# Optimization experiments

Hardware: AMD Instinct MI355X
Metric: run time of the kernel (lower is better)

The kernel has to match this reference:

```python
import jax, jax.numpy as jnp
import numpy as np

K = 16          # nsample (ball-query neighbors via topk smallest sqdist)
EPS = 1e-5      # BatchNorm eps


def conv1(x, W, b):
    # pointwise Conv1d (kernel=1): x [B,N,Cin], W [Cout,Cin], b [Cout] -> [B,N,Cout]
    return jnp.einsum('bnc,oc->bno', x, W) + b


def bn_train(x, gamma, beta):
    # BatchNorm1d in training mode: stats over batch and length dims
    mean = jnp.mean(x, axis=(0, 1))
    var = jnp.var(x, axis=(0, 1))
    return (x - mean) * jax.lax.rsqrt(var + EPS) * gamma + beta


def farthest_point_sample(xyz, npoint):
    # xyz [B,N,3] -> idx [B,npoint]; deterministic start at index 0
    B, N, _ = xyz.shape

    def step(carry, _):
        dist, far = carry                                        # [B,N], [B]
        centroid = jnp.take_along_axis(xyz, far[:, None, None], axis=1)  # [B,1,3]
        d = jnp.sum((xyz - centroid) ** 2, axis=-1)              # [B,N]
        dist = jnp.minimum(dist, d)
        nxt = jnp.argmax(dist, axis=1).astype(jnp.int32)
        return (dist, nxt), far

    init = (jnp.full((B, N), jnp.finfo(xyz.dtype).max, xyz.dtype),
            jnp.zeros((B,), jnp.int32))
    _, idx = jax.lax.scan(step, init, None, length=npoint)       # [npoint,B]
    return idx.T                                                  # [B,npoint]


def sqdist(a, b):
    # a [B,S,3], b [B,N,3] -> [B,S,N]
    return (jnp.sum(a ** 2, -1)[:, :, None]
            + jnp.sum(b ** 2, -1)[:, None, :]
            - 2.0 * jnp.einsum('bsc,bnc->bsn', a, b))


def gather_groups(pc, idx):
    # pc [B,N,D], idx [B,S,K] -> [B,S,K,D]
    return jax.vmap(lambda p, i: p[i])(pc, idx)


def setup_inputs() -> dict:
    key = jax.random.key(0)
    ks = jax.random.split(key, 8)
    B, N = 8, 4096
    mid, out, cin = 32, 64, 3
    s = lambda fan: 1.0 / np.sqrt(fan)
    return {
        'x_in': jax.random.normal(ks[0], (B, N, cin), jnp.float32),
        'W1': jax.random.normal(ks[1], (mid, cin), jnp.float32) * s(cin),
        'b1': jnp.zeros((mid,), jnp.float32),
        'g1': jnp.ones((mid,), jnp.float32),
        'be1': jnp.zeros((mid,), jnp.float32),
        'W2': jax.random.normal(ks[2], (out, mid), jnp.float32) * s(mid),
        'b2': jnp.zeros((out,), jnp.float32),
        'W3': jax.random.normal(ks[3], (out, out + cin), jnp.float32) * s(out + cin),
        'b3': jnp.zeros((out,), jnp.float32),
        'g2': jnp.ones((out,), jnp.float32),
        'be2': jnp.zeros((out,), jnp.float32),
        'W4': jax.random.normal(ks[4], (out, out), jnp.float32) * s(out),
        'b4': jnp.zeros((out,), jnp.float32),
    }


def reference(x_in, W1, b1, g1, be1, W2, b2, W3, b3, g2, be2, W4, b4):
    B, N, C = x_in.shape
    S = N // 2
    # first_mlp: Conv1d -> BN -> ReLU -> Conv1d (all pointwise)
    h = jax.nn.relu(bn_train(conv1(x_in, W1, b1), g1, be1))
    feats = conv1(h, W2, b2)                                  # [B,N,64]
    # sample_and_group(npoint=N//2, nsample=K, xyz=x_in, points=feats)
    fps_idx = farthest_point_sample(x_in, S)                  # [B,S]
    new_xyz = jnp.take_along_axis(x_in, fps_idx[..., None], axis=1)  # [B,S,3]
    d = sqdist(new_xyz, x_in)                                 # [B,S,N]
    _, idx = jax.lax.top_k(-d, K)                             # [B,S,K] smallest dists
    grouped_xyz = gather_groups(x_in, idx) - new_xyz[:, :, None, :]  # [B,S,K,3]
    grouped_pts = gather_groups(feats, idx)                   # [B,S,K,64]
    x_cat = jnp.concatenate([grouped_xyz, grouped_pts], axis=-1)  # [B,S,K,67]
    pooled = jnp.max(x_cat, axis=2)                           # [B,S,67]
    # last_mlp
    h = jax.nn.relu(bn_train(conv1(pooled, W3, b3), g2, be2))
    return conv1(h, W4, b4)                                   # [B,S,64]
```

## Files before the change

### kernel.cpp

```cpp
#include <hip/hip_runtime.h>
#include <float.h>

#define BB   8
#define NN   4096
#define SS   2048
#define MID  32
#define COUT 64
#define CAT  67
#define M1   (BB*NN)
#define M2   (BB*SS)
#define EPSB 1e-5f
#define NCHUNK 64
#define CSZ    32

#define I_B0   0
#define I_B1   16
#define I_B2   32
#define I_TKT  64
#define I_PROG 80
#define WS_RED2  256
#define WS_RED1  400
#define WS_FPS   1024
#define WS_FEATS (1024 + 16384)
#define WS_POOL  (WS_FEATS + M1*COUT)

struct SA  { float red[8][9]; };
struct SB4 { float4 Pc[NN]; alignas(16) unsigned long long sv[2][8]; };
struct SB3 { float W1s[96]; float abv[64]; float W2s[2048]; float b2s[64]; float mom[9]; };
struct SC  { float4 Pq[NN]; unsigned long long cand[CSZ][257]; int fin[CSZ][16];
             float W3s[64 * CAT]; float b3s[64]; float ps[128]; int tkt; };
struct SE  { float W3t[CAT * 64]; float W4s[4096]; float b3s[64]; float b4s[64]; float ab[128]; };
union  SU  { SA a; SB4 b4; SB3 b3; SC c; SE e; };

__device__ __forceinline__ unsigned long long u64max(unsigned long long a,
                                                     unsigned long long b) {
    return a > b ? a : b;
}

template <int CTRL>
__device__ __forceinline__ unsigned long long dpp_swap_max(unsigned long long v) {
    int lo = (int)(unsigned)v;
    int hi = (int)(unsigned)(v >> 32);
    int olo = __builtin_amdgcn_update_dpp(0, lo, CTRL, 0xF, 0xF, false);
    int ohi = __builtin_amdgcn_update_dpp(0, hi, CTRL, 0xF, 0xF, false);
    unsigned long long ov = ((unsigned long long)(unsigned)ohi << 32) | (unsigned)olo;
    return u64max(v, ov);
}

__device__ __forceinline__ void barrier_join(int* ctr, int target) {
    __syncthreads();
    if (threadIdx.x == 0) {
        __threadfence();
        atomicAdd(ctr, 1);
        while (__hip_atomic_load(ctr, __ATOMIC_RELAXED, __HIP_MEMORY_SCOPE_AGENT) < target)
            __builtin_amdgcn_s_sleep(64);
        __threadfence();
    }
    __syncthreads();
}

__device__ __forceinline__ void top16_insert(unsigned long long* cv,
                                             unsigned long long newv,
                                             unsigned long long& cmaxv, int& cpos) {
#pragma unroll
    for (int j = 0; j < 16; j++) cv[j] = (j == cpos) ? newv : cv[j];
    unsigned long long m1a[8]; int p1a[8];
#pragma unroll
    for (int j = 0; j < 8; j++) {
        bool s = cv[2 * j + 1] > cv[2 * j];
        m1a[j] = s ? cv[2 * j + 1] : cv[2 * j];
        p1a[j] = s ? 2 * j + 1 : 2 * j;
    }
    unsigned long long m2a[4]; int p2a[4];
#pragma unroll
    for (int j = 0; j < 4; j++) {
        bool s = m1a[2 * j + 1] > m1a[2 * j];
        m2a[j] = s ? m1a[2 * j + 1] : m1a[2 * j];
        p2a[j] = s ? p1a[2 * j + 1] : p1a[2 * j];
    }
    unsigned long long m3a, m3b; int p3a, p3b;
    { bool s = m2a[1] > m2a[0]; m3a = s ? m2a[1] : m2a[0]; p3a = s ? p2a[1] : p2a[0]; }
    { bool s = m2a[3] > m2a[2]; m3b = s ? m2a[3] : m2a[2]; p3b = s ? p2a[3] : p2a[2]; }
    bool s = m3b > m3a;
    cmaxv = s ? m3b : m3a; cpos = s ? p3b : p3a;
}

__global__ __launch_bounds__(512) void fused(
        const float* __restrict__ xin,
        const float* __restrict__ W1, const float* __restrict__ b1,
        const float* __restrict__ g1, const float* __restrict__ be1,
        const float* __restrict__ W2, const float* __restrict__ b2,
        const float* __restrict__ W3, const float* __restrict__ b3,
        const float* __restrict__ g2, const float* __restrict__ be2,
        const float* __restrict__ W4, const float* __restrict__ b4,
        float* __restrict__ ws, float* __restrict__ out) {
    __shared__ SU sm;
    int blk = blockIdx.x, tid = threadIdx.x;
    int* ctri  = (int*)ws;
    int* fidxg = (int*)(ws + WS_FPS);
    (void)b1;

    if (blk < 8) {
        int b = blk;
        const float* xb = xin + (size_t)b * NN * 3;
        int* fob = fidxg + b * SS;
        int* progb = ctri + I_PROG + b * 16;
        float px[8], py[8], pz[8], dist[8];
#pragma unroll
        for (int k = 0; k < 8; k++) {
            int i = tid + (k << 9);
            float x = xb[3 * i], y = xb[3 * i + 1], z = xb[3 * i + 2];
            px[k] = x; py[k] = y; pz[k] = z; dist[k] = FLT_MAX;
            sm.b4.Pc[i] = make_float4(x, y, z, 0.f);
        }
        __syncthreads();
        float4 c0 = sm.b4.Pc[0];
        float cx = c0.x, cy = c0.y, cz = c0.z;
        int wid = tid >> 6, lane = tid & 63;
        int rbuf[8];
        rbuf[0] = 0;
        for (int t = 1; t < SS; t++) {
            float bv = -1.f; int bi = 0;
#pragma unroll
            for (int k = 0; k < 8; k++) {
                float dx = px[k] - cx, dy = py[k] - cy, dz = pz[k] - cz;
                float d = fmaf(dz, dz, fmaf(dy, dy, dx * dx));
                float nd = fminf(dist[k], d);
                dist[k] = nd;
                bool bt = nd > bv;
                bv = bt ? nd : bv; bi = bt ? (tid + (k << 9)) : bi;
            }
            unsigned long long v =
                ((unsigned long long)__float_as_uint(bv) << 32) | (unsigned)(~bi);
            v = dpp_swap_max<0xB1>(v);
            v = dpp_swap_max<0x4E>(v);
            v = dpp_swap_max<0x141>(v);
            v = dpp_swap_max<0x140>(v);
            {
                int a16 = ((lane ^ 16) << 2), a32 = ((lane ^ 32) << 2), a48 = ((lane ^ 48) << 2);
                int lo = (int)(unsigned)v, hi = (int)(unsigned)(v >> 32);
                int lo16 = __builtin_amdgcn_ds_bpermute(a16, lo);
                int hi16 = __builtin_amdgcn_ds_bpermute(a16, hi);
                int lo32 = __builtin_amdgcn_ds_bpermute(a32, lo);
                int hi32 = __builtin_amdgcn_ds_bpermute(a32, hi);
                int lo48 = __builtin_amdgcn_ds_bpermute(a48, lo);
                int hi48 = __builtin_amdgcn_ds_bpermute(a48, hi);
                unsigned long long v16 = ((unsigned long long)(unsigned)hi16 << 32) | (unsigned)lo16;
                unsigned long long v32 = ((unsigned long long)(unsigned)hi32 << 32) | (unsigned)lo32;
                unsigned long long v48 = ((unsigned long long)(unsigned)hi48 << 32) | (unsigned)lo48;
                v = u64max(u64max(v, v16), u64max(v32, v48));
            }
            int par = t & 1;
            if (lane == 0) sm.b4.sv[par][wid] = v;
            __syncthreads();
            const ulonglong2* sp = (const ulonglong2*)sm.b4.sv[par];
            ulonglong2 q0 = sp[0], q1 = sp[1], q2 = sp[2], q3 = sp[3];
            unsigned long long m0 = u64max(q0.x, q0.y), m1 = u64max(q1.x, q1.y);
            unsigned long long m2 = u64max(q2.x, q2.y), m3 = u64max(q3.x, q3.y);
            unsigned long long best = u64max(u64max(m0, m1), u64max(m2, m3));
            int bsel = (int)(~(unsigned)best);
            float4 cc = sm.b4.Pc[bsel];
            cx = cc.x; cy = cc.y; cz = cc.z;
            if (tid == 0) {
                rbuf[t & 7] = bsel;
                if ((t & 7) == 7) {
                    *(int4*)(fob + t - 7) = make_int4(rbuf[0], rbuf[1], rbuf[2], rbuf[3]);
                    *(int4*)(fob + t - 3) = make_int4(rbuf[4], rbuf[5], rbuf[6], rbuf[7]);
                    if ((t & 31) == 31)
                        __hip_atomic_store(progb, t + 1, __ATOMIC_RELEASE,
                                           __HIP_MEMORY_SCOPE_AGENT);
                }
            }
        }
        barrier_join(ctri + I_B2, 256);
    } else {
        if (blk < 72) {
            int p = (blk - 8) * 512 + tid;
            float x0 = xin[3 * p], x1 = xin[3 * p + 1], x2 = xin[3 * p + 2];
            float r[9];
            r[0] = x0; r[1] = x1; r[2] = x2;
            r[3] = x0 * x0; r[4] = x0 * x1; r[5] = x0 * x2;
            r[6] = x1 * x1; r[7] = x1 * x2; r[8] = x2 * x2;
#pragma unroll
            for (int m = 32; m; m >>= 1) {
#pragma unroll
                for (int q = 0; q < 9; q++) r[q] += __shfl_down(r[q], m, 64);
            }
            if ((tid & 63) == 0) {
#pragma unroll
                for (int q = 0; q < 9; q++) sm.a.red[tid >> 6][q] = r[q];
            }
            __syncthreads();
            if (tid == 0) {
#pragma unroll
                for (int q = 0; q < 9; q++) {
                    float s = 0.f;
#pragma unroll
                    for (int w = 0; w < 8; w++) s += sm.a.red[w][q];
                    ws[WS_RED1 + (blk - 8) * 9 + q] = s;
                }
            }
            barrier_join(ctri + I_B0, 64);
            for (int j = tid; j < 96; j += 512) sm.b3.W1s[j] = W1[j];
            if (tid < 64) sm.b3.b2s[tid] = b2[tid];
            for (int j = tid; j < 2048; j += 512) sm.b3.W2s[j] = W2[j];
            if (tid < 9) {
                float s = 0.f;
                for (int k = 0; k < 64; k++) s += ws[WS_RED1 + k * 9 + tid];
                sm.b3.mom[tid] = s;
            }
            __syncthreads();
            if (tid < MID) {
                float S0 = sm.b3.mom[0], S1 = sm.b3.mom[1], S2 = sm.b3.mom[2];
                float C00 = sm.b3.mom[3], C01 = sm.b3.mom[4], C02 = sm.b3.mom[5];
                float C11 = sm.b3.mom[6], C12 = sm.b3.mom[7], C22 = sm.b3.mom[8];
                float w0 = W1[3 * tid], w1 = W1[3 * tid + 1], w2 = W1[3 * tid + 2];
                float invM = 1.f / (float)M1;
                float meanc = (w0 * S0 + w1 * S1 + w2 * S2) * invM;
                float wCw = w0 * w0 * C00 + w1 * w1 * C11 + w2 * w2 * C22 +
                            2.f * (w0 * w1 * C01 + w0 * w2 * C02 + w1 * w2 * C12);
                float var = wCw * invM - meanc * meanc;
                float a = g1[tid] * rsqrtf(var + EPSB);
                sm.b3.abv[tid] = a;
                sm.b3.abv[MID + tid] = be1[tid] - meanc * a;
            }
            __syncthreads();
            int p2 = (blk - 8) * 512 + tid;
            float y0 = xin[3 * p2], y1 = xin[3 * p2 + 1], y2 = xin[3 * p2 + 2];
            float h[MID];
#pragma unroll
            for (int o = 0; o < MID; o++) {
                float y = fmaf(sm.b3.W1s[3 * o + 2], y2,
                         fmaf(sm.b3.W1s[3 * o + 1], y1, sm.b3.W1s[3 * o] * y0));
                h[o] = fmaxf(0.f, fmaf(sm.b3.abv[o], y, sm.b3.abv[MID + o]));
            }
            float* fo = ws + WS_FEATS + (size_t)p2 * COUT;
#pragma unroll
            for (int j = 0; j < COUT; j += 4) {
                float a0 = sm.b3.b2s[j], a1v = sm.b3.b2s[j + 1];
                float a2v = sm.b3.b2s[j + 2], a3v = sm.b3.b2s[j + 3];
#pragma unroll
                for (int o = 0; o < MID; o++) {
                    float hv = h[o];
                    a0  = fmaf(sm.b3.W2s[(j)     * MID + o], hv, a0);
                    a1v = fmaf(sm.b3.W2s[(j + 1) * MID + o], hv, a1v);
                    a2v = fmaf(sm.b3.W2s[(j + 2) * MID + o], hv, a2v);
                    a3v = fmaf(sm.b3.W2s[(j + 3) * MID + o], hv, a3v);
                }
                *(float4*)(fo + j) = make_float4(a0, a1v, a2v, a3v);
            }
        }
        barrier_join(ctri + I_B1, 248);

        for (int j = tid; j < 64 * CAT; j += 512) sm.c.W3s[j] = W3[j];
        if (tid < 64) sm.c.b3s[tid] = b3[tid];
        if (tid < 128) sm.c.ps[tid] = 0.f;
        __syncthreads();
        int c0ch = (tid & 15) * 4;
        float bsum[4] = {0.f, 0.f, 0.f, 0.f}, bsq[4] = {0.f, 0.f, 0.f, 0.f};
        int curb = -1;
        for (;;) {
            if (tid == 0) sm.c.tkt = atomicAdd(ctri + I_TKT, 1);
            __syncthreads();
            int tk = sm.c.tkt;
            if (tk >= BB * NCHUNK) break;
            int b = tk & 7, c = tk >> 3;
            if (b != curb) {
                const float* xb = xin + (size_t)b * NN * 3;
                for (int j = tid; j < NN; j += 512) {
                    float x = xb[3 * j], y = xb[3 * j + 1], z = xb[3 * j + 2];
                    sm.c.Pq[j] = make_float4(x, y, z, (x * x + y * y) + z * z);
                }
                curb = b;
            }
            if (tid == 0) {
                int* progb = ctri + I_PROG + b * 16;
                int need = (c + 1) * CSZ;
                while (__hip_atomic_load(progb, __ATOMIC_RELAXED,
                                         __HIP_MEMORY_SCOPE_AGENT) < need)
                    __builtin_amdgcn_s_sleep(64);
                (void)__hip_atomic_load(progb, __ATOMIC_ACQUIRE,
                                        __HIP_MEMORY_SCOPE_AGENT);
            }
            __syncthreads();
            int cc = tid >> 4, q = tid & 15;
            int s = c * CSZ + cc;
            int sg = b * SS + s;
            int ci = fidxg[sg];
            float4 cen = sm.c.Pq[ci];
            float an = cen.w;
            unsigned long long cv[16];
#pragma unroll
            for (int j = 0; j < 16; j++) cv[j] = ~0ULL;
            unsigned long long cmaxv = ~0ULL; int cpos = 0;
            for (int n0 = 0; n0 < 256; n0++) {
                int n = (q << 8) + ((n0 + q) & 255);
                float4 qq = sm.c.Pq[n];
                float dot = fmaf(cen.z, qq.z, fmaf(cen.y, qq.y, cen.x * qq.x));
                float dd = (an + qq.w) - 2.f * dot;
                unsigned db = __float_as_uint(dd);
                db ^= (unsigned)(((int)db >> 31) | 0x80000000u);
                unsigned long long newv = ((unsigned long long)db << 32) | (unsigned)n;
                if (newv < cmaxv) top16_insert(cv, newv, cmaxv, cpos);
            }
#pragma unroll
            for (int j = 0; j < 16; j++) sm.c.cand[cc][q * 16 + j] = cv[j];
            __syncthreads();
            if (tid < CSZ) {
                unsigned long long mv[16];
#pragma unroll
                for (int j = 0; j < 16; j++) mv[j] = ~0ULL;
                unsigned long long mx = ~0ULL; int mp = 0;
                for (int k = 0; k < 256; k++) {
                    unsigned long long e = sm.c.cand[tid][k];
                    if (e < mx) top16_insert(mv, e, mx, mp);
                }
#pragma unroll
                for (int j = 0; j < 16; j++) sm.c.fin[tid][j] = (int)(unsigned)mv[j];
            }
            __syncthreads();
            int idxs[16];
#pragma unroll
            for (int j = 0; j < 16; j++) idxs[j] = sm.c.fin[cc][j];
            const float* feats = ws + WS_FEATS + (size_t)b * NN * COUT;
            float4 acc = make_float4(-FLT_MAX, -FLT_MAX, -FLT_MAX, -FLT_MAX);
#pragma unroll 4
            for (int k = 0; k < 16; k++) {
                const float4* fp = (const float4*)(feats + (size_t)idxs[k] * COUT) + q;
                float4 v0 = fp[0];
                acc.x = fmaxf(acc.x, v0.x); acc.y = fmaxf(acc.y, v0.y);
                acc.z = fmaxf(acc.z, v0.z); acc.w = fmaxf(acc.w, v0.w);
            }
            float* po = ws + WS_POOL + (size_t)sg * CAT;
            po[3 + q * 4] = acc.x; po[4 + q * 4] = acc.y;
            po[5 + q * 4] = acc.z; po[6 + q * 4] = acc.w;
            if (q == 0) {
                float rx = -FLT_MAX, ry = -FLT_MAX, rz = -FLT_MAX;
#pragma unroll
                for (int k = 0; k < 16; k++) {
                    float4 p = sm.c.Pq[idxs[k]];
                    rx = fmaxf(rx, p.x - cen.x);
                    ry = fmaxf(ry, p.y - cen.y);
                    rz = fmaxf(rz, p.z - cen.z);
                }
                po[0] = rx; po[1] = ry; po[2] = rz;
            }
            __syncthreads();
            {
                int rrow = b * SS + c * CSZ + (tid >> 4);
                const float* rp = ws + WS_POOL + (size_t)rrow * CAT;
                float y0 = sm.c.b3s[c0ch],     y1 = sm.c.b3s[c0ch + 1];
                float y2 = sm.c.b3s[c0ch + 2], y3 = sm.c.b3s[c0ch + 3];
                for (int j = 0; j < CAT; j++) {
                    float pj = rp[j];
                    y0 = fmaf(sm.c.W3s[(c0ch)     * CAT + j], pj, y0);
                    y1 = fmaf(sm.c.W3s[(c0ch + 1) * CAT + j], pj, y1);
                    y2 = fmaf(sm.c.W3s[(c0ch + 2) * CAT + j], pj, y2);
                    y3 = fmaf(sm.c.W3s[(c0ch + 3) * CAT + j], pj, y3);
                }
                bsum[0] += y0; bsq[0] = fmaf(y0, y0, bsq[0]);
                bsum[1] += y1; bsq[1] = fmaf(y1, y1, bsq[1]);
                bsum[2] += y2; bsq[2] = fmaf(y2, y2, bsq[2]);
                bsum[3] += y3; bsq[3] = fmaf(y3, y3, bsq[3]);
            }
        }
#pragma unroll
        for (int u = 0; u < 4; u++) {
            atomicAdd(&sm.c.ps[c0ch + u], bsum[u]);
            atomicAdd(&sm.c.ps[64 + c0ch + u], bsq[u]);
        }
        __syncthreads();
        if (tid < 128) atomicAdd(ws + WS_RED2 + tid, sm.c.ps[tid]);
        barrier_join(ctri + I_B2, 256);
    }

    {
        for (int lin = tid; lin < CAT * 64; lin += 512) {
            int j = lin >> 6, o = lin & 63;
            sm.e.W3t[lin] = W3[o * CAT + j];
        }
        for (int j = tid; j < 4096; j += 512) sm.e.W4s[j] = W4[j];
        if (tid < 64) {
            sm.e.b3s[tid] = b3[tid]; sm.e.b4s[tid] = b4[tid];
            float inv = 1.f / (float)M2;
            float mean = ws[WS_RED2 + tid] * inv;
            float var = ws[WS_RED2 + 64 + tid] * inv - mean * mean;
            float a = g2[tid] * rsqrtf(var + EPSB);
            sm.e.ab[tid] = a;
            sm.e.ab[64 + tid] = be2[tid] - mean * a;
        }
        __syncthreads();
        if (tid < 64) {
            int pt = blk * 64 + tid;
            const float* row = ws + WS_POOL + (size_t)pt * CAT;
            float h[64];
#pragma unroll
            for (int c = 0; c < 64; c++) h[c] = sm.e.b3s[c];
            for (int j = 0; j < CAT; j++) {
                float pj = row[j];
#pragma unroll
                for (int c = 0; c < 64; c++) h[c] = fmaf(sm.e.W3t[j * 64 + c], pj, h[c]);
            }
#pragma unroll
            for (int c = 0; c < 64; c++)
                h[c] = fmaxf(0.f, fmaf(sm.e.ab[c], h[c], sm.e.ab[64 + c]));
            float* op = out + (size_t)pt * 64;
            for (int o = 0; o < 64; o += 4) {
                float a0 = sm.e.b4s[o], a1v = sm.e.b4s[o + 1];
                float a2v = sm.e.b4s[o + 2], a3v = sm.e.b4s[o + 3];
#pragma unroll
                for (int c = 0; c < 64; c++) {
                    float hv = h[c];
                    a0  = fmaf(sm.e.W4s[(o)     * 64 + c], hv, a0);
                    a1v = fmaf(sm.e.W4s[(o + 1) * 64 + c], hv, a1v);
                    a2v = fmaf(sm.e.W4s[(o + 2) * 64 + c], hv, a2v);
                    a3v = fmaf(sm.e.W4s[(o + 3) * 64 + c], hv, a3v);
                }
                *(float4*)(op + o) = make_float4(a0, a1v, a2v, a3v);
            }
        }
    }
}

extern "C" void kernel_launch(void* const* d_in, const int* in_sizes, int n_in,
                              void* d_out, int out_size, void* d_ws, size_t ws_size,
                              hipStream_t stream) {
    (void)in_sizes; (void)n_in; (void)out_size; (void)ws_size;
    const float* xin = (const float*)d_in[0];
    const float* W1  = (const float*)d_in[1];
    const float* b1  = (const float*)d_in[2];
    const float* g1  = (const float*)d_in[3];
    const float* be1 = (const float*)d_in[4];
    const float* W2  = (const float*)d_in[5];
    const float* b2  = (const float*)d_in[6];
    const float* W3  = (const float*)d_in[7];
    const float* b3  = (const float*)d_in[8];
    const float* g2  = (const float*)d_in[9];
    const float* be2 = (const float*)d_in[10];
    const float* W4  = (const float*)d_in[11];
    const float* b4  = (const float*)d_in[12];
    float* ws  = (float*)d_ws;
    float* out = (float*)d_out;

    hipMemsetAsync(d_ws, 0, 4096, stream);
    void* args[] = {
        (void*)&xin, (void*)&W1, (void*)&b1, (void*)&g1, (void*)&be1,
        (void*)&W2, (void*)&b2, (void*)&W3, (void*)&b3, (void*)&g2,
        (void*)&be2, (void*)&W4, (void*)&b4, (void*)&ws, (void*)&out
    };
    hipLaunchCooperativeKernel((const void*)fused, dim3(256), dim3(512),
                               args, 0, stream);
}
```

Baseline: 2.097 ms.

## Use DPP row broadcasts in FPS reduction and prefetch final weights before barrier

Swaps the ds_bpermute cross-row max in the farthest-point-sampling loop for two DPP row_bcast steps, with lane 63 now writing the wave result, and keeps the index ring buffer in scalar registers instead of an indexed array. The final W3/W4 weight loads move into registers before the grid barrier so their global latency overlaps the wait, and the barrier join is hoisted out of both branches. The top-k candidate write to shared memory is rotated per row to cut bank conflicts. The serial FPS loop dominates, so trimming its per-iteration reduction latency is the main aim; the extra registers could raise pressure.

```diff
diff --git a/kernel.cpp b/kernel.cpp
--- a/kernel.cpp
+++ b/kernel.cpp
@@ -117,8 +117,7 @@
         float4 c0 = sm.b4.Pc[0];
         float cx = c0.x, cy = c0.y, cz = c0.z;
         int wid = tid >> 6, lane = tid & 63;
-        int rbuf[8];
-        rbuf[0] = 0;
+        int r0 = 0, r1 = 0, r2 = 0, r3 = 0, r4 = 0, r5 = 0, r6 = 0, r7 = 0;
         for (int t = 1; t < SS; t++) {
             float bv = -1.f; int bi = 0;
 #pragma unroll
@@ -136,22 +135,10 @@
             v = dpp_swap_max<0x4E>(v);
             v = dpp_swap_max<0x141>(v);
             v = dpp_swap_max<0x140>(v);
-            {
-                int a16 = ((lane ^ 16) << 2), a32 = ((lane ^ 32) << 2), a48 = ((lane ^ 48) << 2);
-                int lo = (int)(unsigned)v, hi = (int)(unsigned)(v >> 32);
-                int lo16 = __builtin_amdgcn_ds_bpermute(a16, lo);
-                int hi16 = __builtin_amdgcn_ds_bpermute(a16, hi);
-                int lo32 = __builtin_amdgcn_ds_bpermute(a32, lo);
-                int hi32 = __builtin_amdgcn_ds_bpermute(a32, hi);
-                int lo48 = __builtin_amdgcn_ds_bpermute(a48, lo);
-                int hi48 = __builtin_amdgcn_ds_bpermute(a48, hi);
-                unsigned long long v16 = ((unsigned long long)(unsigned)hi16 << 32) | (unsigned)lo16;
-                unsigned long long v32 = ((unsigned long long)(unsigned)hi32 << 32) | (unsigned)lo32;
-                unsigned long long v48 = ((unsigned long long)(unsigned)hi48 << 32) | (unsigned)lo48;
-                v = u64max(u64max(v, v16), u64max(v32, v48));
-            }
+            v = dpp_swap_max<0x142>(v);
+            v = dpp_swap_max<0x143>(v);
             int par = t & 1;
-            if (lane == 0) sm.b4.sv[par][wid] = v;
+            if (lane == 63) sm.b4.sv[par][wid] = v;
             __syncthreads();
             const ulonglong2* sp = (const ulonglong2*)sm.b4.sv[par];
             ulonglong2 q0 = sp[0], q1 = sp[1], q2 = sp[2], q3 = sp[3];
@@ -162,17 +149,25 @@
             float4 cc = sm.b4.Pc[bsel];
             cx = cc.x; cy = cc.y; cz = cc.z;
             if (tid == 0) {
-                rbuf[t & 7] = bsel;
+                switch (t & 7) {
+                    case 0: r0 = bsel; break;
+                    case 1: r1 = bsel; break;
+                    case 2: r2 = bsel; break;
+                    case 3: r3 = bsel; break;
+                    case 4: r4 = bsel; break;
+                    case 5: r5 = bsel; break;
+                    case 6: r6 = bsel; break;
+                    default: r7 = bsel; break;
+                }
                 if ((t & 7) == 7) {
-                    *(int4*)(fob + t - 7) = make_int4(rbuf[0], rbuf[1], rbuf[2], rbuf[3]);
-                    *(int4*)(fob + t - 3) = make_int4(rbuf[4], rbuf[5], rbuf[6], rbuf[7]);
+                    *(int4*)(fob + t - 7) = make_int4(r0, r1, r2, r3);
+                    *(int4*)(fob + t - 3) = make_int4(r4, r5, r6, r7);
                     if ((t & 31) == 31)
                         __hip_atomic_store(progb, t + 1, __ATOMIC_RELEASE,
                                            __HIP_MEMORY_SCOPE_AGENT);
                 }
             }
         }
-        barrier_join(ctri + I_B2, 256);
     } else {
         if (blk < 72) {
             int p = (blk - 8) * 512 + tid;
@@ -304,7 +299,8 @@
                 if (newv < cmaxv) top16_insert(cv, newv, cmaxv, cpos);
             }
 #pragma unroll
-            for (int j = 0; j < 16; j++) sm.c.cand[cc][q * 16 + j] = cv[j];
+            for (int j = 0; j < 16; j++)
+                sm.c.cand[cc][q * 16 + ((j + q) & 15)] = cv[j];
             __syncthreads();
             if (tid < CSZ) {
                 unsigned long long mv[16];
@@ -371,15 +367,27 @@
         }
         __syncthreads();
         if (tid < 128) atomicAdd(ws + WS_RED2 + tid, sm.c.ps[tid]);
-        barrier_join(ctri + I_B2, 256);
-    }
+        __syncthreads();
+    }
+
+    float wpre[17];
+#pragma unroll
+    for (int u = 0; u < 9; u++) {
+        int lin = u * 512 + tid;
+        wpre[u] = (lin < CAT * 64) ? W3[(lin & 63) * CAT + (lin >> 6)] : 0.f;
+    }
+#pragma unroll
+    for (int u = 0; u < 8; u++) wpre[9 + u] = W4[u * 512 + tid];
+    barrier_join(ctri + I_B2, 256);
 
     {
-        for (int lin = tid; lin < CAT * 64; lin += 512) {
-            int j = lin >> 6, o = lin & 63;
-            sm.e.W3t[lin] = W3[o * CAT + j];
-        }
-        for (int j = tid; j < 4096; j += 512) sm.e.W4s[j] = W4[j];
+#pragma unroll
+        for (int u = 0; u < 9; u++) {
+            int lin = u * 512 + tid;
+            if (lin < CAT * 64) sm.e.W3t[lin] = wpre[u];
+        }
+#pragma unroll
+        for (int u = 0; u < 8; u++) sm.e.W4s[u * 512 + tid] = wpre[9 + u];
         if (tid < 64) {
             sm.e.b3s[tid] = b3[tid]; sm.e.b4s[tid] = b4[tid];
             float inv = 1.f / (float)M2;
```

Result: slower. 2.315 ms (+10.4%).
